# Kernel tuning notes

Hardware: AMD Instinct MI355X
Metric: run time of the kernel (lower is better)

## Reference

```python
import jax, jax.numpy as jnp
from jax import lax
import numpy as np

B = 64          # batch
HW = 28         # image height/width (hardcoded in module)
LATENT = 256    # latent_size
LABEL = 10      # label_size
FEAT = 64 * HW * HW  # 50176, encoder/decoder fc feature dim


def _conv(x, w, pad):
    # x: [N,C,H,W], w: [O,I,kH,kW]
    return lax.conv_general_dilated(
        x, w, (1, 1), ((pad, pad), (pad, pad)),
        dimension_numbers=('NCHW', 'OIHW', 'NCHW'))


def _conv_transpose(x, w, b, pad):
    # ConvTranspose2d(stride=1, padding=pad) == conv with flipped, transposed
    # kernel and padding k-1-pad. w: [I,O,kH,kW] (torch ConvTranspose layout).
    k = w.shape[2]
    wt = jnp.flip(w, (2, 3)).transpose(1, 0, 2, 3)  # [O,I,kH,kW]
    return _conv(x, wt, k - 1 - pad) + b[None, :, None, None]


def _encoder(images, c1w, c1b, c2w, c2b, fcw, fcb):
    x = jax.nn.relu(_conv(images, c1w, 2) + c1b[None, :, None, None])
    x = jax.nn.relu(_conv(x, c2w, 2) + c2b[None, :, None, None])
    x = x.reshape(x.shape[0], FEAT)
    return jnp.tanh(x @ fcw.T + fcb)


def _decoder(z, fcw, fcb, ct2w, ct2b, ct1w, ct1b):
    x = jnp.arctanh(z)
    x = (x @ fcw.T + fcb).reshape(-1, 64, HW, HW)
    x = jax.nn.relu(_conv_transpose(x, ct2w, ct2b, 2))
    return _conv_transpose(x, ct1w, ct1b, 2)


def _hopfield_weight(patterns):
    # TrainHopfield: Hebbian outer-product sum with mean subtraction,
    # zero diagonal, normalized by number of patterns. One GEMM.
    rho = jnp.mean(patterns)
    t = patterns - rho                      # [L, latent]
    w = t.T @ t                             # [latent, latent]
    w = w - jnp.diag(jnp.diag(w))
    return w / patterns.shape[0]


def _cluster(s0, w):
    # Batched version of: iterate s = sign(w @ s) up to LATENT steps,
    # stopping per-sample when energy -s@w@s stops changing.
    def energy(s):
        return -jnp.einsum('bi,ij,bj->b', s, w, s)

    def step(carry, _):
        s, prev_e, done = carry
        new_s = jnp.sign(s @ w.T)           # w symmetric; per-sample w@s
        e = energy(new_s)
        s_next = jnp.where(done[:, None], s, new_s)
        prev_e_next = jnp.where(done, prev_e, e)
        done_next = done | (e == prev_e)
        return (s_next, prev_e_next, done_next), None

    init = (s0, energy(s0), jnp.zeros(s0.shape[0], dtype=bool))
    (s, _, _), _ = lax.scan(step, init, None, length=LATENT)
    return s


def setup_inputs() -> dict:
    key = jax.random.key(0)
    ks = jax.random.split(key, 12)
    s = 0.05
    f32 = jnp.float32
    return {
        'images': jax.random.normal(ks[0], (B, 1, HW, HW), f32),
        'enc_c1_w': jax.random.normal(ks[1], (32, 1, 5, 5), f32) * s,
        'enc_c1_b': jnp.zeros((32,), f32),
        'enc_c2_w': jax.random.normal(ks[2], (64, 32, 5, 5), f32) * s,
        'enc_c2_b': jnp.zeros((64,), f32),
        'enc_fc_w': jax.random.normal(ks[3], (LATENT, FEAT), f32) * 0.005,
        'enc_fc_b': jnp.zeros((LATENT,), f32),
        'dec_fc_w': jax.random.normal(ks[4], (FEAT, LATENT), f32) * s,
        'dec_fc_b': jnp.zeros((FEAT,), f32),
        'dec_ct2_w': jax.random.normal(ks[5], (64, 32, 5, 5), f32) * s,
        'dec_ct2_b': jnp.zeros((32,), f32),
        'dec_ct1_w': jax.random.normal(ks[6], (32, 1, 5, 5), f32) * s,
        'dec_ct1_b': jnp.zeros((1,), f32),
        'sm_w': jax.random.normal(ks[7], (LABEL, LATENT), f32) * s,
        'sm_b': jnp.zeros((LABEL,), f32),
        'label_latent': jnp.tanh(jax.random.normal(ks[8], (LABEL, LATENT), f32)),
    }


def reference(images, enc_c1_w, enc_c1_b, enc_c2_w, enc_c2_b, enc_fc_w,
              enc_fc_b, dec_fc_w, dec_fc_b, dec_ct2_w, dec_ct2_b, dec_ct1_w,
              dec_ct1_b, sm_w, sm_b, label_latent):
    z = _encoder(images, enc_c1_w, enc_c1_b, enc_c2_w, enc_c2_b,
                 enc_fc_w, enc_fc_b)                       # [B, latent]
    w = _hopfield_weight(jnp.sign(label_latent))           # [latent, latent]
    s0 = lax.stop_gradient(jnp.sign(z))                    # detached copy
    clustered = _cluster(s0, w)                            # [B, latent]
    cluster_probs = jax.nn.softmax(clustered @ label_latent.T, axis=1)
    class_probs = jax.nn.softmax(z @ sm_w.T + sm_b, axis=1)
    recon = _decoder(z, dec_fc_w, dec_fc_b, dec_ct2_w, dec_ct2_b,
                     dec_ct1_w, dec_ct1_b)                 # [B,1,28,28]
    return (cluster_probs, class_probs, recon)
```

## Files before the change

### kernel.cpp

```cpp
#include <hip/hip_runtime.h>
#include <hip/hip_bf16.h>
#include <math.h>

#define BATCH 64
#define HW 28
#define PIX 784
#define LATENT 256
#define LABEL 10
#define FEAT 50176
#define KS 196
#define TSTR 36

typedef __attribute__((ext_vector_type(8))) short bf16x8;
typedef __attribute__((ext_vector_type(4))) float f32x4;

__device__ __forceinline__ float sgnf(float v) {
    return (v > 0.f) ? 1.f : ((v < 0.f) ? -1.f : 0.f);
}

__device__ __forceinline__ short f2bf(float f) {
    union { float f; unsigned u; } v; v.f = f;
    unsigned r = v.u + 0x7FFF + ((v.u >> 16) & 1);
    return (short)(r >> 16);
}
__device__ __forceinline__ float bf2f(short s) {
    union { unsigned u; float f; } v; v.u = ((unsigned)(unsigned short)s) << 16;
    return v.f;
}

__device__ __forceinline__ void split3(const float* __restrict__ p,
                                       bf16x8& h, bf16x8& m, bf16x8& l) {
    float4 a = *(const float4*)p;
    float4 b = *(const float4*)(p + 4);
    float v[8] = {a.x, a.y, a.z, a.w, b.x, b.y, b.z, b.w};
    #pragma unroll
    for (int j = 0; j < 8; ++j) {
        short s0 = f2bf(v[j]); float r = v[j] - bf2f(s0);
        short s1 = f2bf(r);    float r2 = r - bf2f(s1);
        h[j] = s0; m[j] = s1; l[j] = f2bf(r2);
    }
}

template<int G, int FLIP>
__global__ __launch_bounds__(256) void conv5_k(const float* __restrict__ in,
                        const float* __restrict__ w,
                        const float* __restrict__ bias, float* __restrict__ out,
                        int IC, int OC, int relu) {
    int b = blockIdx.x, oc0 = blockIdx.y * G;
    __shared__ float plp[2][32 * TSTR];
    int tid = threadIdx.x;

    for (int t = tid; t < 2 * 32 * TSTR; t += 256) ((float*)plp)[t] = 0.f;

    bool actS = tid < 196;
    int ys = tid / 7, qs = tid % 7;

    int q = tid & 7, yy = tid >> 3;
    bool actC = (q < 7) && (yy < 28);
    int x0 = q * 4;

    float acc[G][4];
    #pragma unroll
    for (int g = 0; g < G; ++g)
        #pragma unroll
        for (int xi = 0; xi < 4; ++xi) acc[g][xi] = 0.f;

    __syncthreads();
    if (actS) {
        float4 v = *(const float4*)&in[((size_t)(b * IC + 0)) * PIX + tid * 4];
        *(float2*)&plp[0][(ys + 2) * TSTR + 4 * qs + 2] = make_float2(v.x, v.y);
        *(float2*)&plp[0][(ys + 2) * TSTR + 4 * qs + 4] = make_float2(v.z, v.w);
    }
    __syncthreads();

    for (int ic = 0; ic < IC; ++ic) {
        float4 vn;
        bool more = (ic + 1) < IC;
        if (more && actS)
            vn = *(const float4*)&in[((size_t)(b * IC + ic + 1)) * PIX + tid * 4];

        const float* tile = plp[ic & 1];
        if (actC) {
            #pragma unroll
            for (int dy = 0; dy < 5; ++dy) {
                float4 ra = *(const float4*)&tile[(yy + dy) * TSTR + x0];
                float4 rb = *(const float4*)&tile[(yy + dy) * TSTR + x0 + 4];
                float rw[8] = {ra.x, ra.y, ra.z, ra.w, rb.x, rb.y, rb.z, rb.w};
                #pragma unroll
                for (int g = 0; g < G; ++g) {
                    #pragma unroll
                    for (int dx = 0; dx < 5; ++dx) {
                        float wv = FLIP
                            ? w[((size_t)ic * OC + (oc0 + g)) * 25 + (4 - dy) * 5 + (4 - dx)]
                            : w[((size_t)(oc0 + g) * IC + ic) * 25 + dy * 5 + dx];
                        #pragma unroll
                        for (int xi = 0; xi < 4; ++xi)
                            acc[g][xi] += rw[xi + dx] * wv;
                    }
                }
            }
        }
        if (more && actS) {
            float* nt = plp[(ic + 1) & 1];
            *(float2*)&nt[(ys + 2) * TSTR + 4 * qs + 2] = make_float2(vn.x, vn.y);
            *(float2*)&nt[(ys + 2) * TSTR + 4 * qs + 4] = make_float2(vn.z, vn.w);
        }
        __syncthreads();
    }

    if (actC) {
        #pragma unroll
        for (int g = 0; g < G; ++g) {
            float bv = bias[oc0 + g];
            float4 o;
            o.x = acc[g][0] + bv;
            o.y = acc[g][1] + bv;
            o.z = acc[g][2] + bv;
            o.w = acc[g][3] + bv;
            if (relu) {
                o.x = fmaxf(o.x, 0.f); o.y = fmaxf(o.y, 0.f);
                o.z = fmaxf(o.z, 0.f); o.w = fmaxf(o.w, 0.f);
            }
            *(float4*)&out[((size_t)(b * OC + (oc0 + g))) * PIX + yy * HW + x0] = o;
        }
    }
}

__global__ __launch_bounds__(64, 1) void c2_mfma_k(const short* __restrict__ xh,
                        const short* __restrict__ xm, const short* __restrict__ xl,
                        const short* __restrict__ wb,
                        const float* __restrict__ bias, float* __restrict__ out) {
    int b = blockIdx.x;
    int t0 = blockIdx.y * 4;
    int lane = threadIdx.x;
    int prow = lane & 15, kgrp = lane >> 4;

    f32x4 acc[4][4];
    #pragma unroll
    for (int pt = 0; pt < 4; ++pt)
        #pragma unroll
        for (int nt = 0; nt < 4; ++nt) acc[pt][nt] = (f32x4){0.f, 0.f, 0.f, 0.f};

    int py[4], px[4];
    bool ptv[4];
    #pragma unroll
    for (int pt = 0; pt < 4; ++pt) {
        int p = (t0 + pt) * 16 + prow;
        ptv[pt] = (t0 + pt) < 49;
        py[pt] = p / 28; px[pt] = p % 28;
    }

    const bf16x8 zero8 = {0,0,0,0,0,0,0,0};
    #pragma unroll 5
    for (int tap = 0; tap < 25; ++tap) {
        int dy = tap / 5 - 2, dx = tap % 5 - 2;
        const short* wt = wb + (size_t)tap * 2048;
        bf16x8 B0[4], B1[4], B2[4];
        #pragma unroll
        for (int nt = 0; nt < 4; ++nt) {
            int off = (nt * 16 + prow) * 32 + kgrp * 8;
            B0[nt] = *(const bf16x8*)&wt[off];
            B1[nt] = *(const bf16x8*)&wt[51200 + off];
            B2[nt] = *(const bf16x8*)&wt[102400 + off];
        }
        #pragma unroll
        for (int pt = 0; pt < 4; ++pt) {
            int ysrc = py[pt] + dy, xsrc = px[pt] + dx;
            bool valid = ptv[pt] && (ysrc >= 0) && (ysrc < 28) && (xsrc >= 0) && (xsrc < 28);
            int yc = min(max(ysrc, 0), 27), xc = min(max(xsrc, 0), 27);
            size_t o = ((size_t)b * PIX + yc * 28 + xc) * 32 + kgrp * 8;
            bf16x8 ah = *(const bf16x8*)&xh[o];
            bf16x8 am = *(const bf16x8*)&xm[o];
            bf16x8 al = *(const bf16x8*)&xl[o];
            if (!valid) { ah = zero8; am = zero8; al = zero8; }
            #pragma unroll
            for (int nt = 0; nt < 4; ++nt) {
                acc[pt][nt] = __builtin_amdgcn_mfma_f32_16x16x32_bf16(ah, B0[nt], acc[pt][nt], 0, 0, 0);
                acc[pt][nt] = __builtin_amdgcn_mfma_f32_16x16x32_bf16(ah, B1[nt], acc[pt][nt], 0, 0, 0);
                acc[pt][nt] = __builtin_amdgcn_mfma_f32_16x16x32_bf16(am, B0[nt], acc[pt][nt], 0, 0, 0);
                acc[pt][nt] = __builtin_amdgcn_mfma_f32_16x16x32_bf16(ah, B2[nt], acc[pt][nt], 0, 0, 0);
                acc[pt][nt] = __builtin_amdgcn_mfma_f32_16x16x32_bf16(am, B1[nt], acc[pt][nt], 0, 0, 0);
                acc[pt][nt] = __builtin_amdgcn_mfma_f32_16x16x32_bf16(al, B0[nt], acc[pt][nt], 0, 0, 0);
            }
        }
    }

    __shared__ float ot[64][17];
    float bv = bias[lane];
    for (int pt = 0; pt < 4; ++pt) {
        if (!ptv[pt]) continue;
        #pragma unroll
        for (int nt = 0; nt < 4; ++nt)
            #pragma unroll
            for (int r = 0; r < 4; ++r)
                ot[nt * 16 + prow][kgrp * 4 + r] = acc[pt][nt][r];
        float* op = &out[((size_t)(b * 64 + lane)) * PIX + (t0 + pt) * 16];
        #pragma unroll
        for (int i = 0; i < 4; ++i) {
            float4 o;
            o.x = fmaxf(ot[lane][i * 4 + 0] + bv, 0.f);
            o.y = fmaxf(ot[lane][i * 4 + 1] + bv, 0.f);
            o.z = fmaxf(ot[lane][i * 4 + 2] + bv, 0.f);
            o.w = fmaxf(ot[lane][i * 4 + 3] + bv, 0.f);
            *(float4*)&op[i * 4] = o;
        }
    }
}

__global__ void xsplit3_k(const float* __restrict__ x, short* __restrict__ xh,
                          short* __restrict__ xm, short* __restrict__ xl) {
    __shared__ float lds[32][17];
    int b = blockIdx.x, pbase = blockIdx.y * 16;
    int t = threadIdx.x;
    if (t < 128) {
        int ic = t >> 2, pj = (t & 3) * 4;
        float4 v = *(const float4*)&x[((size_t)(b * 32 + ic)) * PIX + pbase + pj];
        lds[ic][pj + 0] = v.x; lds[ic][pj + 1] = v.y;
        lds[ic][pj + 2] = v.z; lds[ic][pj + 3] = v.w;
    }
    __syncthreads();
    int p = t >> 4, ic2 = (t & 15) * 2;
    size_t o = ((size_t)b * PIX + pbase + p) * 32 + ic2;
    short2 h, m, l;
    {
        float v = lds[ic2][p];
        short s0 = f2bf(v); float r = v - bf2f(s0);
        short s1 = f2bf(r); float r2 = r - bf2f(s1);
        h.x = s0; m.x = s1; l.x = f2bf(r2);
    }
    {
        float v = lds[ic2 + 1][p];
        short s0 = f2bf(v); float r = v - bf2f(s0);
        short s1 = f2bf(r); float r2 = r - bf2f(s1);
        h.y = s0; m.y = s1; l.y = f2bf(r2);
    }
    *(short2*)&xh[o] = h;
    *(short2*)&xm[o] = m;
    *(short2*)&xl[o] = l;
}

__global__ void wprep3_k(const float* __restrict__ w, short* __restrict__ wb) {
    int j = blockIdx.x * 256 + threadIdx.x;
    if (j < 51200) {
        int ic = j & 31;
        int oc = (j >> 5) & 63;
        int tap = j >> 11;
        float v = w[((size_t)oc * 32 + ic) * 25 + tap];
        short s0 = f2bf(v); float r = v - bf2f(s0);
        short s1 = f2bf(r); float r2 = r - bf2f(s1);
        wb[j] = s0;
        wb[51200 + j] = s1;
        wb[102400 + j] = f2bf(r2);
    }
}

__global__ __launch_bounds__(64, 1) void ct2_mfma_k(const short* __restrict__ xb,
                        const short* __restrict__ wb,
                        const float* __restrict__ bias, float* __restrict__ out) {
    int b = blockIdx.x;
    int pbase = blockIdx.y * 16;
    int lane = threadIdx.x;
    int prow = lane & 15;
    int kgrp = lane >> 4;
    int p = pbase + prow;
    int py = p / 28, px = p % 28;

    f32x4 acc0 = {0.f, 0.f, 0.f, 0.f};
    f32x4 acc1 = {0.f, 0.f, 0.f, 0.f};

    const bf16x8 zero8 = {0,0,0,0,0,0,0,0};
    #pragma unroll 5
    for (int tap = 0; tap < 25; ++tap) {
        int dy = tap / 5 - 2, dx = tap % 5 - 2;
        int ysrc = py + dy, xsrc = px + dx;
        bool valid = (ysrc >= 0) && (ysrc < 28) && (xsrc >= 0) && (xsrc < 28);
        int yc = min(max(ysrc, 0), 27), xc = min(max(xsrc, 0), 27);

        const bf16x8* ap = (const bf16x8*)&xb[((size_t)b * PIX + yc * 28 + xc) * 64 + kgrp * 8];
        bf16x8 a0 = ap[0];
        bf16x8 a1 = ap[4];
        if (!valid) { a0 = zero8; a1 = zero8; }
        const short* wt = &wb[(size_t)tap * 32 * 64];
        int oc_l = lane & 15;
        bf16x8 b00 = *(const bf16x8*)&wt[oc_l * 64 + kgrp * 8];
        bf16x8 b01 = *(const bf16x8*)&wt[oc_l * 64 + 32 + kgrp * 8];
        bf16x8 b10 = *(const bf16x8*)&wt[(16 + oc_l) * 64 + kgrp * 8];
        bf16x8 b11 = *(const bf16x8*)&wt[(16 + oc_l) * 64 + 32 + kgrp * 8];

        acc0 = __builtin_amdgcn_mfma_f32_16x16x32_bf16(a0, b00, acc0, 0, 0, 0);
        acc0 = __builtin_amdgcn_mfma_f32_16x16x32_bf16(a1, b01, acc0, 0, 0, 0);
        acc1 = __builtin_amdgcn_mfma_f32_16x16x32_bf16(a0, b10, acc1, 0, 0, 0);
        acc1 = __builtin_amdgcn_mfma_f32_16x16x32_bf16(a1, b11, acc1, 0, 0, 0);
    }

    __shared__ float ot[32][16];
    int drow = (lane >> 4) * 4;
    #pragma unroll
    for (int r = 0; r < 4; ++r) {
        ot[lane & 15][drow + r]        = acc0[r];
        ot[16 + (lane & 15)][drow + r] = acc1[r];
    }
    __syncthreads();
    int oc = lane >> 1, ph = (lane & 1) * 8;
    float bv = bias[oc];
    float4 o0, o1;
    o0.x = fmaxf(ot[oc][ph + 0] + bv, 0.f);
    o0.y = fmaxf(ot[oc][ph + 1] + bv, 0.f);
    o0.z = fmaxf(ot[oc][ph + 2] + bv, 0.f);
    o0.w = fmaxf(ot[oc][ph + 3] + bv, 0.f);
    o1.x = fmaxf(ot[oc][ph + 4] + bv, 0.f);
    o1.y = fmaxf(ot[oc][ph + 5] + bv, 0.f);
    o1.z = fmaxf(ot[oc][ph + 6] + bv, 0.f);
    o1.w = fmaxf(ot[oc][ph + 7] + bv, 0.f);
    float* op = &out[((size_t)(b * 32 + oc)) * PIX + pbase + ph];
    *(float4*)&op[0] = o0;
    *(float4*)&op[4] = o1;
}

__global__ void wprep_k(const float* __restrict__ w, short* __restrict__ wb) {
    int j = blockIdx.x * 256 + threadIdx.x;
    if (j < 25 * 32 * 64) {
        int ic = j & 63;
        int oc = (j >> 6) & 31;
        int tap = j >> 11;
        int dyi = tap / 5, dxi = tap % 5;
        wb[j] = f2bf(w[((size_t)ic * 32 + oc) * 25 + (4 - dyi) * 5 + (4 - dxi)]);
    }
}

__global__ void xpose16_k(const short* __restrict__ y16, short* __restrict__ xb) {
    __shared__ short lds[64][16];
    int b = blockIdx.x, pbase = blockIdx.y * 16;
    int t = threadIdx.x;
    {
        int ic = t >> 2, pj = (t & 3) * 4;
        short4 v = *(const short4*)&y16[((size_t)(b * 64 + ic)) * PIX + pbase + pj];
        lds[ic][pj + 0] = v.x;
        lds[ic][pj + 1] = v.y;
        lds[ic][pj + 2] = v.z;
        lds[ic][pj + 3] = v.w;
    }
    __syncthreads();
    {
        int p = t >> 4, icq = (t & 15) * 4;
        short4 s;
        s.x = lds[icq + 0][p];
        s.y = lds[icq + 1][p];
        s.z = lds[icq + 2][p];
        s.w = lds[icq + 3][p];
        *(short4*)&xb[((size_t)b * PIX + pbase + p) * 64 + icq] = s;
    }
}

__global__ __launch_bounds__(512) void enc_fc_mfma_k(const float* __restrict__ x,
                        const float* __restrict__ w,
                        float* __restrict__ pA, float* __restrict__ pB) {
    int ks = blockIdx.x;
    int nh = blockIdx.y;
    int kbase = ks * 256;
    int tid = threadIdx.x;
    int lane = tid & 63, wv = tid >> 6;
    int prow = lane & 15, kgrp = lane >> 4;
    int nrow = nh * 128 + wv * 16 + prow;

    f32x4 acc[4];
    #pragma unroll
    for (int mt = 0; mt < 4; ++mt) acc[mt] = (f32x4){0.f, 0.f, 0.f, 0.f};

    for (int kt = 0; kt < 8; ++kt) {
        int kof = kbase + kt * 32 + kgrp * 8;
        bf16x8 bh, bm, bl;
        split3(&w[(size_t)nrow * FEAT + kof], bh, bm, bl);
        #pragma unroll
        for (int mt = 0; mt < 4; ++mt) {
            bf16x8 ah, am, al;
            split3(&x[(size_t)(mt * 16 + prow) * FEAT + kof], ah, am, al);
            acc[mt] = __builtin_amdgcn_mfma_f32_16x16x32_bf16(ah, bh, acc[mt], 0, 0, 0);
            acc[mt] = __builtin_amdgcn_mfma_f32_16x16x32_bf16(ah, bm, acc[mt], 0, 0, 0);
            acc[mt] = __builtin_amdgcn_mfma_f32_16x16x32_bf16(am, bh, acc[mt], 0, 0, 0);
            acc[mt] = __builtin_amdgcn_mfma_f32_16x16x32_bf16(ah, bl, acc[mt], 0, 0, 0);
            acc[mt] = __builtin_amdgcn_mfma_f32_16x16x32_bf16(am, bm, acc[mt], 0, 0, 0);
            acc[mt] = __builtin_amdgcn_mfma_f32_16x16x32_bf16(al, bh, acc[mt], 0, 0, 0);
        }
    }

    __shared__ float ot[64 * 129];
    #pragma unroll
    for (int mt = 0; mt < 4; ++mt)
        #pragma unroll
        for (int r = 0; r < 4; ++r) {
            int m = mt * 16 + kgrp * 4 + r;
            ot[m * 129 + wv * 16 + prow] = acc[mt][r];
        }
    __syncthreads();
    float* base = (ks < 98) ? (pA + (size_t)ks * BATCH * LATENT)
                            : (pB + (size_t)(ks - 98) * BATCH * LATENT);
    int m = tid >> 3, c0 = (tid & 7) * 4;
    float* pp = &base[m * 256 + nh * 128];
    #pragma unroll
    for (int i = 0; i < 4; ++i) {
        int n = c0 + i * 32;
        *(float4*)&pp[n] = *(float4*)&ot[m * 129 + n];
    }
}

__global__ void enc_fc_fin_k(const float* __restrict__ pA, const float* __restrict__ pB,
                             const float* __restrict__ bias,
                             float* __restrict__ z, short* __restrict__ xah,
                             short* __restrict__ xam) {
    int m = blockIdx.x;
    int n = threadIdx.x;
    int idx = m * 256 + n;
    float a = bias[n];
    for (int ksi = 0; ksi < 98; ++ksi) a += pA[(size_t)ksi * BATCH * LATENT + idx];
    for (int ksi = 0; ksi < 98; ++ksi) a += pB[(size_t)ksi * BATCH * LATENT + idx];
    float zv = tanhf(a);
    z[idx] = zv;
    float xv = atanhf(zv);
    short h = f2bf(xv);
    xah[idx] = h;
    xam[idx] = f2bf(xv - bf2f(h));
}

__global__ void hop_rho_k(const float* __restrict__ ll, float* __restrict__ rho_out) {
    float p = 0.f;
    for (int t = threadIdx.x; t < LABEL * LATENT; t += 256) p += sgnf(ll[t]);
    __shared__ float red[8];
    for (int o = 32; o; o >>= 1) p += __shfl_down(p, o, 64);
    if ((threadIdx.x & 63) == 0) red[threadIdx.x >> 6] = p;
    __syncthreads();
    if (threadIdx.x == 0)
        rho_out[0] = (red[0] + red[1] + red[2] + red[3]) / (float)(LABEL * LATENT);
}

__global__ void hop_w_k(const float* __restrict__ ll, const float* __restrict__ rho_p,
                        float* __restrict__ wout) {
    int i = blockIdx.x, j = threadIdx.x;
    float rho = rho_p[0];
    float acc = 0.f;
    #pragma unroll
    for (int l = 0; l < LABEL; ++l) {
        float a = sgnf(ll[l * LATENT + i]) - rho;
        float b = sgnf(ll[l * LATENT + j]) - rho;
        acc += a * b;
    }
    wout[i * LATENT + j] = (i == j) ? 0.f : acc / 10.f;
}

__global__ __launch_bounds__(1024) void cluster_k(const float* __restrict__ z,
                          const float* __restrict__ w,
                          const float* __restrict__ ll, float* __restrict__ out) {
    int b = blockIdx.x;
    int t = threadIdx.x;
    int i = t & 255;
    int q = t >> 8;
    int lane = t & 63;
    int wvid = t >> 6;

    __shared__ float s_sh[LATENT];
    __shared__ float part[1024];
    __shared__ float red[4];
    __shared__ float cflag[4];
    __shared__ int ctl_sh;
    __shared__ float logit[LABEL];

    float wreg[64];
    #pragma unroll
    for (int jj = 0; jj < 64; ++jj)
        wreg[jj] = w[(q * 64 + jj) * LATENT + i];

    float s_cur = 0.f, s_old = 2.f, v = 0.f;
    float e_prev = 0.f;
    if (q == 0) {
        s_cur = sgnf(z[b * LATENT + i]);
        s_sh[i] = s_cur;
    }
    __syncthreads();

    {
        float p0 = 0.f, p1 = 0.f;
        #pragma unroll
        for (int jj = 0; jj < 64; jj += 2) {
            p0 += wreg[jj]     * s_sh[q * 64 + jj];
            p1 += wreg[jj + 1] * s_sh[q * 64 + jj + 1];
        }
        part[t] = p0 + p1;
    }
    __syncthreads();
    if (q == 0) {
        v = part[i] + part[i + 256] + part[i + 512] + part[i + 768];
        float p = s_cur * v;
        #pragma unroll
        for (int o = 32; o; o >>= 1) p += __shfl_down(p, o, 64);
        if (lane == 0) red[wvid] = p;
    }
    __syncthreads();
    if (t == 0) e_prev = -(red[0] + red[1] + red[2] + red[3]);

    for (int it = 0; it < LATENT; ++it) {
        if (q == 0) {
            float ns = sgnf(v);
            unsigned long long m = __ballot(ns == s_old);
            if (lane == 0) cflag[wvid] = (m == ~0ull) ? 1.f : 0.f;
            s_sh[i] = ns;
            s_old = s_cur;
            s_cur = ns;
        }
        __syncthreads();
        {
            float p0 = 0.f, p1 = 0.f;
            #pragma unroll
            for (int jj = 0; jj < 64; jj += 2) {
                p0 += wreg[jj]     * s_sh[q * 64 + jj];
                p1 += wreg[jj + 1] * s_sh[q * 64 + jj + 1];
            }
            part[t] = p0 + p1;
        }
        __syncthreads();
        if (q == 0) {
            v = part[i] + part[i + 256] + part[i + 512] + part[i + 768];
            float p = s_cur * v;
            #pragma unroll
            for (int o = 32; o; o >>= 1) p += __shfl_down(p, o, 64);
            if (lane == 0) red[wvid] = p;
        }
        __syncthreads();
        if (t == 0) {
            float e = -(red[0] + red[1] + red[2] + red[3]);
            int c = 0;
            if (e == e_prev) c = 1;
            else if (it >= 1 && cflag[0] != 0.f && cflag[1] != 0.f &&
                     cflag[2] != 0.f && cflag[3] != 0.f)
                c = (((LATENT - 1 - it) & 1) == 0) ? 2 : 3;
            else e_prev = e;
            ctl_sh = c;
        }
        __syncthreads();
        int c = ctl_sh;
        if (c != 0) {
            if (c == 3 && q == 0) s_sh[i] = s_old;
            break;
        }
    }
    __syncthreads();

    if (wvid < LABEL) {
        float p = 0.f;
        #pragma unroll
        for (int r = 0; r < 4; ++r)
            p += s_sh[r * 64 + lane] * ll[wvid * LATENT + r * 64 + lane];
        #pragma unroll
        for (int o = 32; o; o >>= 1) p += __shfl_down(p, o, 64);
        if (lane == 0) logit[wvid] = p;
    }
    __syncthreads();
    if (t == 0) {
        float mx = logit[0];
        for (int c = 1; c < LABEL; ++c) mx = fmaxf(mx, logit[c]);
        float ex[LABEL];
        float s = 0.f;
        for (int c = 0; c < LABEL; ++c) { ex[c] = expf(logit[c] - mx); s += ex[c]; }
        for (int c = 0; c < LABEL; ++c) out[b * LABEL + c] = ex[c] / s;
    }
}

__device__ __forceinline__ float block_sum256(float p, float* red) {
    __syncthreads();
    for (int o = 32; o; o >>= 1) p += __shfl_down(p, o, 64);
    if ((threadIdx.x & 63) == 0) red[threadIdx.x >> 6] = p;
    __syncthreads();
    return red[0] + red[1] + red[2] + red[3];
}

__global__ void class_k(const float* __restrict__ z, const float* __restrict__ smw,
                        const float* __restrict__ smb, float* __restrict__ out) {
    int b = blockIdx.x;
    int i = threadIdx.x;
    __shared__ float red[8];
    __shared__ float logit[LABEL];
    float zi = z[b * LATENT + i];
    for (int c = 0; c < LABEL; ++c) {
        float p = zi * smw[c * LATENT + i];
        float t = block_sum256(p, red);
        if (i == 0) logit[c] = t + smb[c];
    }
    __syncthreads();
    if (i == 0) {
        float mx = logit[0];
        for (int c = 1; c < LABEL; ++c) mx = fmaxf(mx, logit[c]);
        float ex[LABEL];
        float s = 0.f;
        for (int c = 0; c < LABEL; ++c) { ex[c] = expf(logit[c] - mx); s += ex[c]; }
        for (int c = 0; c < LABEL; ++c) out[b * LABEL + c] = ex[c] / s;
    }
}

__global__ __launch_bounds__(256) void dec_fc_mfma_k(const short* __restrict__ xah,
                         const short* __restrict__ xam,
                         const float* __restrict__ w,
                         const float* __restrict__ bias, short* __restrict__ y16) {
    int tid = threadIdx.x;
    int lane = tid & 63, wv = tid >> 6;
    int prow = lane & 15, kgrp = lane >> 4;
    int n0 = blockIdx.x * 64;
    int nb = n0 + wv * 16;

    f32x4 acc[4];
    #pragma unroll
    for (int mi = 0; mi < 4; ++mi) acc[mi] = (f32x4){0.f, 0.f, 0.f, 0.f};

    for (int kc = 0; kc < 8; ++kc) {
        int kof = kc * 32 + kgrp * 8;
        const float* wp = &w[(size_t)(nb + prow) * LATENT + kof];
        float4 w0 = *(const float4*)&wp[0];
        float4 w1 = *(const float4*)&wp[4];
        bf16x8 bf;
        bf[0] = f2bf(w0.x); bf[1] = f2bf(w0.y); bf[2] = f2bf(w0.z); bf[3] = f2bf(w0.w);
        bf[4] = f2bf(w1.x); bf[5] = f2bf(w1.y); bf[6] = f2bf(w1.z); bf[7] = f2bf(w1.w);
        #pragma unroll
        for (int mi = 0; mi < 4; ++mi) {
            bf16x8 ah = *(const bf16x8*)&xah[(mi * 16 + prow) * LATENT + kof];
            bf16x8 am = *(const bf16x8*)&xam[(mi * 16 + prow) * LATENT + kof];
            acc[mi] = __builtin_amdgcn_mfma_f32_16x16x32_bf16(ah, bf, acc[mi], 0, 0, 0);
            acc[mi] = __builtin_amdgcn_mfma_f32_16x16x32_bf16(am, bf, acc[mi], 0, 0, 0);
        }
    }

    __shared__ short ot[64 * 72];
    float bv = bias[nb + prow];
    #pragma unroll
    for (int mi = 0; mi < 4; ++mi)
        #pragma unroll
        for (int r = 0; r < 4; ++r) {
            int m = mi * 16 + kgrp * 4 + r;
            ot[m * 72 + wv * 16 + prow] = f2bf(acc[mi][r] + bv);
        }
    __syncthreads();
    int m = tid >> 2, q = tid & 3;
    #pragma unroll
    for (int i = 0; i < 2; ++i) {
        *(int4*)&y16[(size_t)m * FEAT + n0 + i * 32 + q * 8] =
            *(int4*)&ot[m * 72 + i * 32 + q * 8];
    }
}

extern "C" void kernel_launch(void* const* d_in, const int* in_sizes, int n_in,
                              void* d_out, int out_size, void* d_ws, size_t ws_size,
                              hipStream_t stream) {
    const float* images   = (const float*)d_in[0];
    const float* c1w      = (const float*)d_in[1];
    const float* c1b      = (const float*)d_in[2];
    const float* c2w      = (const float*)d_in[3];
    const float* c2b      = (const float*)d_in[4];
    const float* efw      = (const float*)d_in[5];
    const float* efb      = (const float*)d_in[6];
    const float* dfw      = (const float*)d_in[7];
    const float* dfb      = (const float*)d_in[8];
    const float* ct2w     = (const float*)d_in[9];
    const float* ct2b     = (const float*)d_in[10];
    const float* ct1w     = (const float*)d_in[11];
    const float* ct1b     = (const float*)d_in[12];
    const float* smw      = (const float*)d_in[13];
    const float* smb      = (const float*)d_in[14];
    const float* ll       = (const float*)d_in[15];

    float* out = (float*)d_out;
    float* ws  = (float*)d_ws;

    float* big0 = ws;
    float* big1 = ws + 3211264;
    float* z    = ws + 3211264 + 1605632 + 458752;
    float* whop = z + BATCH * LATENT;
    float* rho  = whop + LATENT * LATENT;
    float* xsa  = rho + 4;
    short* xah  = (short*)xsa;
    short* xam  = xah + 16384;
    short* xbf  = (short*)(xsa + 16384);
    short* wbf  = (short*)(xsa + 16384 + 1605632);
    short* xh3  = xbf;
    short* xm3  = xbf + 1605632;
    short* xl3  = (short*)(xsa + 16384 + 1605632 + 25600);
    short* wb3  = xl3 + 1605632;
    short* y16  = (short*)big0;
    float* partA = big1;
    float* partB = (float*)xbf;

    conv5_k<4,0><<<dim3(BATCH, 8), 256, 0, stream>>>(images, c1w, c1b, big1, 1, 32, 1);
    wprep3_k<<<200, 256, 0, stream>>>(c2w, wb3);
    xsplit3_k<<<dim3(BATCH, 49), 256, 0, stream>>>(big1, xh3, xm3, xl3);
    c2_mfma_k<<<dim3(BATCH, 13), 64, 0, stream>>>(xh3, xm3, xl3, wb3, c2b, big0);
    enc_fc_mfma_k<<<dim3(KS, 2), 512, 0, stream>>>(big0, efw, partA, partB);
    enc_fc_fin_k<<<BATCH, 256, 0, stream>>>(partA, partB, efb, z, xah, xam);

    hop_rho_k<<<1, 256, 0, stream>>>(ll, rho);
    hop_w_k<<<LATENT, 256, 0, stream>>>(ll, rho, whop);
    cluster_k<<<BATCH, 1024, 0, stream>>>(z, whop, ll, out);
    class_k<<<BATCH, 256, 0, stream>>>(z, smw, smb, out + 640);

    wprep_k<<<200, 256, 0, stream>>>(ct2w, wbf);
    dec_fc_mfma_k<<<FEAT / 64, 256, 0, stream>>>(xah, xam, dfw, dfb, y16);
    xpose16_k<<<dim3(BATCH, 49), 256, 0, stream>>>(y16, xbf);
    ct2_mfma_k<<<dim3(BATCH, 49), 64, 0, stream>>>(xbf, wbf, ct2b, big1);
    conv5_k<1,1><<<dim3(BATCH, 1), 256, 0, stream>>>(big1, ct1w, ct1b, out + 1280, 32, 1, 0);
}
```

Before: 305.1 us.

## Stage conv2 input halo tile in LDS and split taps across four waves

The conv2 MFMA kernel now uses 256 threads per block. It first loads a zero-padded halo tile of the three bf16 input limbs into shared memory, which replaces the per-tap global loads with their boundary clamping. The 25 taps are split across four waves, and the partial accumulators are reduced through LDS before the bias+ReLU store. This adds parallelism to a grid of only 832 single-wave blocks and improves input reuse. In exchange it uses about 60KB of LDS per block and adds an extra reduction and synchronisation step.

```diff
diff --git a/kernel.cpp b/kernel.cpp
--- a/kernel.cpp
+++ b/kernel.cpp
@@ -126,14 +126,46 @@
     }
 }
 
-__global__ __launch_bounds__(64, 1) void c2_mfma_k(const short* __restrict__ xh,
+__global__ __launch_bounds__(256) void c2_mfma_k(const short* __restrict__ xh,
                         const short* __restrict__ xm, const short* __restrict__ xl,
                         const short* __restrict__ wb,
                         const float* __restrict__ bias, float* __restrict__ out) {
     int b = blockIdx.x;
-    int t0 = blockIdx.y * 4;
-    int lane = threadIdx.x;
+    int tb = blockIdx.y;
+    int tid = threadIdx.x;
+    int wv4 = tid >> 6;
+    int lane = tid & 63;
     int prow = lane & 15, kgrp = lane >> 4;
+
+    __shared__ __align__(16) char lds_buf[61440];
+    short* atile = (short*)lds_buf;
+    float* red   = (float*)lds_buf;
+    float* ot    = (float*)(lds_buf + 49152);
+
+    int rows_base = (tb * 64) / 28 - 2;
+
+    {
+        int4 z4 = make_int4(0, 0, 0, 0);
+        for (int j = tid; j < 3840; j += 256)
+            ((int4*)lds_buf)[j] = z4;
+    }
+    __syncthreads();
+
+    for (int j = tid; j < 2688; j += 256) {
+        int limb = j / 896;
+        int rem = j % 896;
+        int lr = rem / 112;
+        int ch = rem % 112;
+        int col = ch >> 2, ico = (ch & 3) * 8;
+        int gr = rows_base + lr;
+        if (gr >= 0 && gr < 28) {
+            const short* lp = (limb == 0) ? xh : ((limb == 1) ? xm : xl);
+            const int4* src = (const int4*)&lp[((size_t)(b * PIX + gr * 28 + col)) * 32 + ico];
+            int4* dst = (int4*)&atile[(((size_t)limb * 8 + lr) * 32 + 2 + col) * 40 + ico];
+            *dst = *src;
+        }
+    }
+    __syncthreads();
 
     f32x4 acc[4][4];
     #pragma unroll
@@ -145,14 +177,12 @@
     bool ptv[4];
     #pragma unroll
     for (int pt = 0; pt < 4; ++pt) {
-        int p = (t0 + pt) * 16 + prow;
-        ptv[pt] = (t0 + pt) < 49;
+        int p = (tb * 4 + pt) * 16 + prow;
+        ptv[pt] = (tb * 4 + pt) < 49;
         py[pt] = p / 28; px[pt] = p % 28;
     }
 
-    const bf16x8 zero8 = {0,0,0,0,0,0,0,0};
-    #pragma unroll 5
-    for (int tap = 0; tap < 25; ++tap) {
+    for (int tap = wv4; tap < 25; tap += 4) {
         int dy = tap / 5 - 2, dx = tap % 5 - 2;
         const short* wt = wb + (size_t)tap * 2048;
         bf16x8 B0[4], B1[4], B2[4];
@@ -165,14 +195,12 @@
         }
         #pragma unroll
         for (int pt = 0; pt < 4; ++pt) {
-            int ysrc = py[pt] + dy, xsrc = px[pt] + dx;
-            bool valid = ptv[pt] && (ysrc >= 0) && (ysrc < 28) && (xsrc >= 0) && (xsrc < 28);
-            int yc = min(max(ysrc, 0), 27), xc = min(max(xsrc, 0), 27);
-            size_t o = ((size_t)b * PIX + yc * 28 + xc) * 32 + kgrp * 8;
-            bf16x8 ah = *(const bf16x8*)&xh[o];
-            bf16x8 am = *(const bf16x8*)&xm[o];
-            bf16x8 al = *(const bf16x8*)&xl[o];
-            if (!valid) { ah = zero8; am = zero8; al = zero8; }
+            int lrow = py[pt] + dy - rows_base;
+            int lcol = px[pt] + dx + 2;
+            int aoff = ((lrow * 32 + lcol) * 40) + kgrp * 8;
+            bf16x8 ah = *(const bf16x8*)&atile[aoff];
+            bf16x8 am = *(const bf16x8*)&atile[10240 + aoff];
+            bf16x8 al = *(const bf16x8*)&atile[20480 + aoff];
             #pragma unroll
             for (int nt = 0; nt < 4; ++nt) {
                 acc[pt][nt] = __builtin_amdgcn_mfma_f32_16x16x32_bf16(ah, B0[nt], acc[pt][nt], 0, 0, 0);
@@ -185,24 +213,51 @@
         }
     }
 
-    __shared__ float ot[64][17];
-    float bv = bias[lane];
-    for (int pt = 0; pt < 4; ++pt) {
-        if (!ptv[pt]) continue;
-        #pragma unroll
-        for (int nt = 0; nt < 4; ++nt)
+    __syncthreads();
+    if (wv4 > 0) {
+        float* rw = red + (size_t)(wv4 - 1) * 64 * 64 + (size_t)lane * 64;
+        #pragma unroll
+        for (int pt = 0; pt < 4; ++pt)
             #pragma unroll
-            for (int r = 0; r < 4; ++r)
-                ot[nt * 16 + prow][kgrp * 4 + r] = acc[pt][nt][r];
-        float* op = &out[((size_t)(b * 64 + lane)) * PIX + (t0 + pt) * 16];
-        #pragma unroll
-        for (int i = 0; i < 4; ++i) {
-            float4 o;
-            o.x = fmaxf(ot[lane][i * 4 + 0] + bv, 0.f);
-            o.y = fmaxf(ot[lane][i * 4 + 1] + bv, 0.f);
-            o.z = fmaxf(ot[lane][i * 4 + 2] + bv, 0.f);
-            o.w = fmaxf(ot[lane][i * 4 + 3] + bv, 0.f);
-            *(float4*)&op[i * 4] = o;
+            for (int nt = 0; nt < 4; ++nt)
+                #pragma unroll
+                for (int r = 0; r < 4; ++r)
+                    rw[pt * 16 + nt * 4 + r] = acc[pt][nt][r];
+    }
+    __syncthreads();
+    if (wv4 == 0) {
+        #pragma unroll
+        for (int pt = 0; pt < 4; ++pt)
+            #pragma unroll
+            for (int nt = 0; nt < 4; ++nt)
+                #pragma unroll
+                for (int r = 0; r < 4; ++r) {
+                    int ix = pt * 16 + nt * 4 + r;
+                    float s = acc[pt][nt][r];
+                    s += red[(size_t)0 * 4096 + lane * 64 + ix];
+                    s += red[(size_t)1 * 4096 + lane * 64 + ix];
+                    s += red[(size_t)2 * 4096 + lane * 64 + ix];
+                    acc[pt][nt][r] = s;
+                }
+
+        float bv = bias[lane];
+        for (int pt = 0; pt < 4; ++pt) {
+            if (!ptv[pt]) continue;
+            #pragma unroll
+            for (int nt = 0; nt < 4; ++nt)
+                #pragma unroll
+                for (int r = 0; r < 4; ++r)
+                    ot[(nt * 16 + prow) * 17 + kgrp * 4 + r] = acc[pt][nt][r];
+            float* op = &out[((size_t)(b * 64 + lane)) * PIX + (tb * 4 + pt) * 16];
+            #pragma unroll
+            for (int i = 0; i < 4; ++i) {
+                float4 o;
+                o.x = fmaxf(ot[lane * 17 + i * 4 + 0] + bv, 0.f);
+                o.y = fmaxf(ot[lane * 17 + i * 4 + 1] + bv, 0.f);
+                o.z = fmaxf(ot[lane * 17 + i * 4 + 2] + bv, 0.f);
+                o.w = fmaxf(ot[lane * 17 + i * 4 + 3] + bv, 0.f);
+                *(float4*)&op[i * 4] = o;
+            }
         }
     }
 }
@@ -688,7 +743,7 @@
     conv5_k<4,0><<<dim3(BATCH, 8), 256, 0, stream>>>(images, c1w, c1b, big1, 1, 32, 1);
     wprep3_k<<<200, 256, 0, stream>>>(c2w, wb3);
     xsplit3_k<<<dim3(BATCH, 49), 256, 0, stream>>>(big1, xh3, xm3, xl3);
-    c2_mfma_k<<<dim3(BATCH, 13), 64, 0, stream>>>(xh3, xm3, xl3, wb3, c2b, big0);
+    c2_mfma_k<<<dim3(BATCH, 13), 256, 0, stream>>>(xh3, xm3, xl3, wb3, c2b, big0);
     enc_fc_mfma_k<<<dim3(KS, 2), 512, 0, stream>>>(big0, efw, partA, partB);
     enc_fc_fin_k<<<BATCH, 256, 0, stream>>>(partA, partB, efb, z, xah, xam);
 
```

Measured after the change: 305.1 us. About the same (+0.0%).
